# Optimization experiments

Measured on AMD Instinct MI355X. Metric: run time of the kernel, lower is better.

## Reference

```python
import jax, jax.numpy as jnp
import numpy as np

B, L, H, F, K, NBINS, T = 32, 512, 512, 512, 3, 256, 4096
EPS = 1e-8  # RMSNorm epsilon
PAD = (K - 1) // 2  # =1, matches both conv paddings in the torch module


def _conv1d(x, w, b):
    # x: [B, L, Cin], w: [K, Cin, Cout]
    return jax.lax.conv_general_dilated(
        x, w, window_strides=(1,), padding=[(PAD, PAD)],
        dimension_numbers=('NLC', 'LIO', 'NLC')) + b


def _rms(x, g):
    return g * x / (jnp.sqrt(jnp.mean(x * x, axis=-1, keepdims=True)) + EPS)


def _vpred(x, mask, w1, b1, g1, w2, b2, g2, wl, bl):
    h = _rms(jax.nn.relu(_conv1d(x, w1, b1)), g1)
    h = _rms(jax.nn.relu(_conv1d(h, w2, b2)), g2)
    out = (h @ wl + bl)[..., 0]  # [B, L]
    return jnp.where(mask, 0.0, out)


def _proj(x, w1, b1, w2, b2):
    return jax.nn.relu(jax.nn.relu(x @ w1 + b1) @ w2 + b2)


def _length_regulate(x, dur, max_len):
    # Vectorized equivalent of LengthRegulator: repeat phoneme i dur[b,i] times, pad to max_len.
    cum = jnp.cumsum(dur, axis=1)               # [B, L]
    mel_len = cum[:, -1]                        # [B]
    t = jnp.arange(max_len)                     # [T]
    idx = jax.vmap(lambda c: jnp.searchsorted(c, t, side='right'))(cum)  # [B, T]
    idx = jnp.minimum(idx, x.shape[1] - 1)
    out = jnp.take_along_axis(x, idx[:, :, None], axis=1)  # [B, T, H]
    valid = (t[None, :] < mel_len[:, None])
    return out * valid[:, :, None].astype(x.dtype), mel_len


def setup_inputs() -> dict:
    key = jax.random.key(0)
    ks = iter(jax.random.split(key, 64))
    n = lambda *s: jax.random.normal(next(ks), s, jnp.float32) * 0.05
    inp = {}
    inp['x'] = jax.random.normal(next(ks), (B, L, H), jnp.float32)
    inp['embedding'] = jax.random.normal(next(ks), (B, L, H), jnp.float32)
    inp['src_mask'] = jnp.zeros((B, L), bool)
    inp['duration_target'] = jax.random.randint(next(ks), (B, L), 0, 9, jnp.int32)
    inp['pitch_target'] = jax.random.normal(next(ks), (B, L), jnp.float32)
    inp['energy_target'] = jax.random.normal(next(ks), (B, L), jnp.float32)
    inp['max_len'] = T
    for p in ['dur', 'pit', 'eng']:
        inp[p + '_w1'] = n(K, H, F); inp[p + '_b1'] = jnp.zeros(F, jnp.float32)
        inp[p + '_g1'] = jnp.ones(F, jnp.float32)
        inp[p + '_w2'] = n(K, F, F); inp[p + '_b2'] = jnp.zeros(F, jnp.float32)
        inp[p + '_g2'] = jnp.ones(F, jnp.float32)
        inp[p + '_wl'] = n(F, 1); inp[p + '_bl'] = jnp.zeros(1, jnp.float32)
    for p in ['pp', 'ep', 'sp']:
        inp[p + '_w1'] = n(H, H); inp[p + '_b1'] = jnp.zeros(H, jnp.float32)
        inp[p + '_w2'] = n(H, H); inp[p + '_b2'] = jnp.zeros(H, jnp.float32)
    inp['pitch_bins'] = jnp.linspace(-3.0, 3.0, NBINS - 1)
    inp['energy_bins'] = jnp.linspace(-3.0, 3.0, NBINS - 1)
    inp['pitch_emb'] = n(NBINS, H)
    inp['energy_emb'] = n(NBINS, H)
    return inp


def reference(x, embedding, src_mask, duration_target, pitch_target, energy_target, max_len,
              dur_w1, dur_b1, dur_g1, dur_w2, dur_b2, dur_g2, dur_wl, dur_bl,
              pit_w1, pit_b1, pit_g1, pit_w2, pit_b2, pit_g2, pit_wl, pit_bl,
              eng_w1, eng_b1, eng_g1, eng_w2, eng_b2, eng_g2, eng_wl, eng_bl,
              pp_w1, pp_b1, pp_w2, pp_b2,
              ep_w1, ep_b1, ep_w2, ep_b2,
              sp_w1, sp_b1, sp_w2, sp_b2,
              pitch_bins, energy_bins, pitch_emb, energy_emb):
    log_dur = _vpred(x, src_mask, dur_w1, dur_b1, dur_g1, dur_w2, dur_b2, dur_g2, dur_wl, dur_bl)
    pit_pred = _vpred(x + _proj(embedding, pp_w1, pp_b1, pp_w2, pp_b2), src_mask,
                      pit_w1, pit_b1, pit_g1, pit_w2, pit_b2, pit_g2, pit_wl, pit_bl)
    pitch_embedding = pitch_emb[jnp.searchsorted(pitch_bins, pitch_target)]  # torch.bucketize right=False == side='left'
    eng_pred = _vpred(x + _proj(embedding, ep_w1, ep_b1, ep_w2, ep_b2), src_mask,
                      eng_w1, eng_b1, eng_g1, eng_w2, eng_b2, eng_g2, eng_wl, eng_bl)
    energy_embedding = energy_emb[jnp.searchsorted(energy_bins, energy_target)]
    xo = x + energy_embedding + pitch_embedding + _proj(embedding, sp_w1, sp_b1, sp_w2, sp_b2)
    out, mel_len = _length_regulate(xo, duration_target, max_len)
    return (out, pit_pred, eng_pred, log_dur, mel_len)
```

## Files before the change

### kernel.cpp

```cpp
#include <hip/hip_runtime.h>

#define Bv    32
#define Lv    512
#define Hv    512
#define Fv    512
#define Tv    4096
#define Mv    (Bv*Lv)
#define NBINSv 256

#define OUT_OFF 0
#define PIT_OFF (Bv*(size_t)Tv*Hv)
#define ENG_OFF (PIT_OFF + Mv)
#define DUR_OFF (ENG_OFF + Mv)
#define MEL_OFF (DUR_OFF + Mv)

typedef unsigned short ushort;
typedef __attribute__((ext_vector_type(8))) short   bf16x8;
typedef __attribute__((ext_vector_type(4))) float   f32x4;
typedef __attribute__((ext_vector_type(8))) unsigned short u16x8;

__device__ __forceinline__ float b2f(ushort u) {
    union { float f; unsigned u; } x; x.u = ((unsigned)u) << 16; return x.f;
}
__device__ __forceinline__ ushort f2b(float f) {
    union { float f; unsigned u; } x; x.f = f;
    unsigned r = x.u + 0x7fffu + ((x.u >> 16) & 1u);
    return (ushort)(r >> 16);
}

#define GLL16(g, l) __builtin_amdgcn_global_load_lds( \
    (const __attribute__((address_space(1))) void*)(g), \
    (__attribute__((address_space(3))) void*)(l), 16, 0, 0)

template<int NZ> struct GArgs {
    const ushort* A[NZ];
    const ushort* W[NZ];
    const float*  bias[NZ];
    ushort*       C[NZ];
};
struct EpiArgs {
    float* rss; const float* inv1; float* ss2; float* sgw;
    const float* g2[3]; const float* wl[3];
};
struct TransArgs { const float* src[6]; const float* gs[6]; ushort* dst[6]; };
struct ConvArgs  { const float* src[2]; ushort* dst[2]; };

template<int NTAPS, int EPI, int NZ>
__global__ __launch_bounds__(256) void gemm_bf16_kernel(
    GArgs<NZ> ga, EpiArgs ea, const float* __restrict__ res,
    const float* __restrict__ pe, const float* __restrict__ ee,
    const int* __restrict__ idxp, const int* __restrict__ idxe,
    const ushort* __restrict__ zp)
{
    constexpr int KTOT = NTAPS * 512;
    constexpr int GX   = Fv / 128;
    constexpr int GY   = Mv / 128;
    constexpr int NWG  = GX * GY * NZ;

    int lin = blockIdx.x + GX * (blockIdx.y + GY * blockIdx.z);
    lin = (lin & 7) * (NWG >> 3) + (lin >> 3);
    const int bx = lin & (GX - 1);
    const int by = (lin >> 2) & (GY - 1);
    const int z  = (NZ > 1) ? (lin / (GX * GY)) : 0;

    const ushort* __restrict__ A    = ga.A[z];
    const ushort* __restrict__ Bt   = ga.W[z];
    const float*  __restrict__ bias = ga.bias[z];
    ushort*       __restrict__ C    = ga.C[z];

    __shared__ ushort As[128 * 32];
    __shared__ ushort Bs[128 * 32];

    const int tid = threadIdx.x;
    const int n0 = bx * 128;
    const int m0 = by * 128;

    const int sar = tid >> 2;
    const int sl  = tid & 3;

    const int lane = tid & 63;
    const int w    = tid >> 6;
    const int wm   = (w & 1) * 64;
    const int wn   = (w >> 1) * 64;
    const int lr   = lane & 15;
    const int q    = lane >> 4;

    f32x4 acc[4][4];
    #pragma unroll
    for (int i = 0; i < 4; ++i)
        #pragma unroll
        for (int j = 0; j < 4; ++j) {
            f32x4 zz = {0.f, 0.f, 0.f, 0.f};
            acc[i][j] = zz;
        }

    for (int kt = 0; kt < NTAPS * 16; ++kt) {
        const int tap = (NTAPS == 3) ? (kt >> 4) : 0;
        const int kin = (NTAPS == 3) ? ((kt & 15) << 5) : (kt << 5);

        #pragma unroll
        for (int r = 0; r < 2; ++r) {
            const int row = sar + r * 64;
            const int m   = m0 + row;
            const int qg  = (sl - (row >> 1)) & 3;
            const ushort* asrc;
            if (NTAPS == 3) {
                const int l  = m & (Lv - 1);
                const int ls = l + tap - 1;
                asrc = ((unsigned)ls < (unsigned)Lv)
                     ? A + (size_t)(m + tap - 1) * 512 + kin + qg * 8
                     : zp;
            } else {
                asrc = A + (size_t)m * 512 + kin + qg * 8;
            }
            GLL16(asrc, &As[row * 32 + sl * 8]);
            const ushort* bsrc = Bt + (size_t)(n0 + row) * KTOT + tap * 512 + kin + qg * 8;
            GLL16(bsrc, &Bs[row * 32 + sl * 8]);
        }
        __syncthreads();

        bf16x8 af[4], bfr[4];
        #pragma unroll
        for (int i = 0; i < 4; ++i) {
            const int rm = wm + i * 16 + lr;
            af[i]  = *(const bf16x8*)&As[rm * 32 + (((q + (rm >> 1)) & 3) << 3)];
            const int rn = wn + i * 16 + lr;
            bfr[i] = *(const bf16x8*)&Bs[rn * 32 + (((q + (rn >> 1)) & 3) << 3)];
        }
        #pragma unroll
        for (int i = 0; i < 4; ++i)
            #pragma unroll
            for (int j = 0; j < 4; ++j)
                acc[i][j] = __builtin_amdgcn_mfma_f32_16x16x32_bf16(
                                af[i], bfr[j], acc[i][j], 0, 0, 0);
        __syncthreads();
    }

    int epi = EPI;
    if (EPI == 3) epi = (z == 2) ? 2 : 1;
    #pragma unroll
    for (int i = 0; i < 4; ++i) {
        #pragma unroll
        for (int r = 0; r < 4; ++r) {
            const int m = m0 + wm + i * 16 + q * 4 + r;
            const size_t ro = (size_t)m * 512;
            int ip = 0, ie = 0;
            if (EPI == 3 && epi == 2) { ip = idxp[m]; ie = idxe[m]; }
            float rowinv = 1.f;
            if (EPI == 5) rowinv = ea.inv1[(size_t)z * Mv + m];
            float ssp = 0.f, sgwp = 0.f;
            #pragma unroll
            for (int j = 0; j < 4; ++j) {
                const int n = n0 + wn + j * 16 + lr;
                float v = (EPI == 5) ? (acc[i][j][r] * rowinv + bias[n])
                                     : (acc[i][j][r] + bias[n]);
                v = fmaxf(v, 0.f);
                if (EPI == 3) v += res[ro + n];
                if (EPI == 3 && epi == 2)
                    v += pe[(size_t)ip * 512 + n] + ee[(size_t)ie * 512 + n];
                if (EPI != 5) C[ro + n] = f2b(v);
                if (EPI == 4) ssp += v * v;
                if (EPI == 5) { ssp += v * v; sgwp += v * ea.g2[z][n] * ea.wl[z][n]; }
            }
            if (EPI == 4 || EPI == 5) {
                #pragma unroll
                for (int mm = 1; mm < 16; mm <<= 1) {
                    ssp += __shfl_xor(ssp, mm, 64);
                    if (EPI == 5) sgwp += __shfl_xor(sgwp, mm, 64);
                }
                if (lr == 0) {
                    if (EPI == 4) atomicAdd(&ea.rss[(size_t)z * Mv + m], ssp);
                    if (EPI == 5) {
                        atomicAdd(&ea.ss2[(size_t)z * Mv + m], ssp);
                        atomicAdd(&ea.sgw[(size_t)z * Mv + m], sgwp);
                    }
                }
            }
        }
    }
}

__global__ __launch_bounds__(256) void convert_kernel(ConvArgs ca)
{
    const float* __restrict__ X  = ca.src[blockIdx.y];
    ushort*      __restrict__ Xb = ca.dst[blockIdx.y];
    const size_t i = (size_t)blockIdx.x * 256 + threadIdx.x;
    const float4 a = ((const float4*)X)[2 * i];
    const float4 b = ((const float4*)X)[2 * i + 1];
    u16x8 o;
    o[0] = f2b(a.x); o[1] = f2b(a.y); o[2] = f2b(a.z); o[3] = f2b(a.w);
    o[4] = f2b(b.x); o[5] = f2b(b.y); o[6] = f2b(b.z); o[7] = f2b(b.w);
    *(u16x8*)(Xb + i * 8) = o;
}

__global__ __launch_bounds__(256) void transpose_kernel(TransArgs ta, int Ktot)
{
    const float* __restrict__ W  = ta.src[blockIdx.z];
    const float* __restrict__ gs = ta.gs[blockIdx.z];
    ushort*      __restrict__ Wt = ta.dst[blockIdx.z];
    __shared__ float t[32][33];
    const int k0 = blockIdx.x * 32, n0 = blockIdx.y * 32;
    const int r = threadIdx.x >> 5, c = threadIdx.x & 31;
    #pragma unroll
    for (int rr = 0; rr < 4; ++rr) {
        const int kk = k0 + r + rr * 8;
        float v = W[(size_t)kk * 512 + n0 + c];
        if (gs) v *= gs[kk & 511];
        t[r + rr * 8][c] = v;
    }
    __syncthreads();
    #pragma unroll
    for (int rr = 0; rr < 4; ++rr)
        Wt[(size_t)(n0 + r + rr * 8) * Ktot + k0 + c] = f2b(t[c][r + rr * 8]);
}

__global__ __launch_bounds__(256) void finv_kernel(
    const float* __restrict__ rss, float* __restrict__ inv1)
{
    const int i = blockIdx.x * 256 + threadIdx.x;
    inv1[i] = 1.f / (sqrtf(rss[i] * (1.f / 512.f)) + 1e-8f);
}

__global__ __launch_bounds__(256) void pred_kernel(
    const float* __restrict__ ss2, const float* __restrict__ sgw,
    const unsigned char* __restrict__ mask,
    const float* __restrict__ bl0, const float* __restrict__ bl1,
    const float* __restrict__ bl2, float* __restrict__ predbase)
{
    const int i = blockIdx.x * 256 + threadIdx.x;
    const int zz = i >> 14;
    const int row = i & (Mv - 1);
    const float bl = (zz == 0 ? bl0 : (zz == 1 ? bl1 : bl2))[0];
    const float inv = 1.f / (sqrtf(ss2[i] * (1.f / 512.f)) + 1e-8f);
    predbase[i] = mask[row] ? 0.f : (sgw[i] * inv + bl);
}

__global__ __launch_bounds__(256) void idx_kernel(
    const float* __restrict__ pt, const float* __restrict__ et,
    const float* __restrict__ pbins, const float* __restrict__ ebins,
    int* __restrict__ idxp, int* __restrict__ idxe)
{
    __shared__ float pb[NBINSv - 1], ebn[NBINSv - 1];
    const int tid = threadIdx.x;
    if (tid < NBINSv - 1) { pb[tid] = pbins[tid]; ebn[tid] = ebins[tid]; }
    __syncthreads();
    const int m = blockIdx.x * 256 + tid;
    const float pv = pt[m], ev = et[m];
    int lo = 0, hi = NBINSv - 1;
    while (lo < hi) { int mid = (lo + hi) >> 1; if (pb[mid] < pv) lo = mid + 1; else hi = mid; }
    idxp[m] = lo;
    lo = 0; hi = NBINSv - 1;
    while (lo < hi) { int mid = (lo + hi) >> 1; if (ebn[mid] < ev) lo = mid + 1; else hi = mid; }
    idxe[m] = lo;
}

__global__ __launch_bounds__(512) void cumsum_kernel(
    const int* __restrict__ dur, int* __restrict__ cum,
    int* __restrict__ melint, float* __restrict__ melout)
{
    __shared__ int s[Lv];
    const int b = blockIdx.x, tid = threadIdx.x;
    s[tid] = dur[b * Lv + tid];
    __syncthreads();
    for (int off = 1; off < Lv; off <<= 1) {
        int t = (tid >= off) ? s[tid - off] : 0;
        __syncthreads();
        s[tid] += t;
        __syncthreads();
    }
    cum[b * Lv + tid] = s[tid];
    if (tid == Lv - 1) { melint[b] = s[tid]; melout[b] = (float)s[tid]; }
}

__global__ __launch_bounds__(256) void tmap_kernel(
    const int* __restrict__ cum, const int* __restrict__ melint,
    int* __restrict__ tmap)
{
    const int bt = blockIdx.x * 256 + threadIdx.x;
    const int b = bt >> 12;
    const int t = bt & (Tv - 1);
    const int* c = cum + b * Lv;
    int lo = 0, hi = Lv;
    while (lo < hi) { int mid = (lo + hi) >> 1; if (c[mid] <= t) lo = mid + 1; else hi = mid; }
    tmap[bt] = (t < melint[b]) ? (b * Lv + min(lo, Lv - 1)) : -1;
}

__global__ __launch_bounds__(128) void regulate_kernel(
    const ushort* __restrict__ xo, const int* __restrict__ tmap,
    float* __restrict__ out)
{
    const int bt = blockIdx.x;
    const int src = tmap[bt];
    float4 v = make_float4(0.f, 0.f, 0.f, 0.f);
    if (src >= 0) {
        const ushort4 u = ((const ushort4*)(xo + (size_t)src * 512))[threadIdx.x];
        v.x = b2f(u.x); v.y = b2f(u.y); v.z = b2f(u.z); v.w = b2f(u.w);
    }
    ((float4*)(out + (size_t)bt * 512))[threadIdx.x] = v;
}

extern "C" void kernel_launch(void* const* d_in, const int* in_sizes, int n_in,
                              void* d_out, int out_size, void* d_ws, size_t ws_size,
                              hipStream_t stream)
{
    const float* x    = (const float*)d_in[0];
    const float* emb  = (const float*)d_in[1];
    const unsigned char* mask = (const unsigned char*)d_in[2];
    const int*   durt = (const int*)d_in[3];
    const float* pt   = (const float*)d_in[4];
    const float* et   = (const float*)d_in[5];
    const float* dw1 = (const float*)d_in[7],  *db1 = (const float*)d_in[8],
               * dg1 = (const float*)d_in[9],  *dw2 = (const float*)d_in[10],
               * db2 = (const float*)d_in[11], *dg2 = (const float*)d_in[12],
               * dwl = (const float*)d_in[13], *dbl = (const float*)d_in[14];
    const float* pw1 = (const float*)d_in[15], *pb1 = (const float*)d_in[16],
               * pg1 = (const float*)d_in[17], *pw2 = (const float*)d_in[18],
               * pb2 = (const float*)d_in[19], *pg2 = (const float*)d_in[20],
               * pwl = (const float*)d_in[21], *pbl = (const float*)d_in[22];
    const float* ew1 = (const float*)d_in[23], *eb1 = (const float*)d_in[24],
               * eg1 = (const float*)d_in[25], *ew2 = (const float*)d_in[26],
               * eb2 = (const float*)d_in[27], *eg2 = (const float*)d_in[28],
               * ewl = (const float*)d_in[29], *ebl = (const float*)d_in[30];
    const float* ppw1 = (const float*)d_in[31], *ppb1 = (const float*)d_in[32],
               * ppw2 = (const float*)d_in[33], *ppb2 = (const float*)d_in[34];
    const float* epw1 = (const float*)d_in[35], *epb1 = (const float*)d_in[36],
               * epw2 = (const float*)d_in[37], *epb2 = (const float*)d_in[38];
    const float* spw1 = (const float*)d_in[39], *spb1 = (const float*)d_in[40],
               * spw2 = (const float*)d_in[41], *spb2 = (const float*)d_in[42];
    const float* pbins = (const float*)d_in[43];
    const float* ebins = (const float*)d_in[44];
    const float* pemb  = (const float*)d_in[45];
    const float* eemb  = (const float*)d_in[46];

    float* outf = (float*)d_out;

    int*    cum    = (int*)d_ws;
    int*    melint = cum + 16384;
    int*    idxp   = melint + 64;
    int*    idxe   = idxp + 16384;
    ushort* zp     = (ushort*)(idxe + 16384);
    int*    tmap   = idxe + 16448;
    ushort* xob    = (ushort*)((float*)d_ws + 262144);

    #define OBUF(i) ((ushort*)(outf + (size_t)(i) * 4194304))
    ushort* xb  = OBUF(0);   ushort* eb  = OBUF(1);
    ushort* pA0 = OBUF(2);   ushort* pA1 = OBUF(3);  ushort* pA2 = OBUF(4);
    ushort* xp  = OBUF(5);   ushort* xe  = OBUF(6);
    ushort* c0  = OBUF(7);   ushort* c1  = OBUF(8);  ushort* c2  = OBUF(9);
    float*  rss  = outf + 10ull * 4194304;
    float*  ss2  = rss + 3 * Mv;
    float*  sgw  = rss + 6 * Mv;
    float*  inv1 = rss + 9 * Mv;
    ushort* wt[12];
    {
        size_t off = 13ull * 4194304;
        for (int i = 0; i < 6; ++i)  { wt[i] = (ushort*)(outf + off); off += 393216; }
        for (int i = 6; i < 12; ++i) { wt[i] = (ushort*)(outf + off); off += 131072; }
    }

    hipMemsetAsync(zp, 0, 64, stream);
    hipMemsetAsync(rss, 0, 9ull * Mv * sizeof(float), stream);

    { ConvArgs ca = {{x, emb}, {xb, eb}};
      convert_kernel<<<dim3(4096, 2), 256, 0, stream>>>(ca); }
    { TransArgs ta = {{dw1, dw2, pw1, pw2, ew1, ew2},
                      {nullptr, dg1, nullptr, pg1, nullptr, eg1},
                      {wt[0], wt[1], wt[2], wt[3], wt[4], wt[5]}};
      transpose_kernel<<<dim3(48, 16, 6), 256, 0, stream>>>(ta, 1536); }
    { TransArgs ta = {{ppw1, ppw2, epw1, epw2, spw1, spw2},
                      {nullptr, nullptr, nullptr, nullptr, nullptr, nullptr},
                      {wt[6], wt[7], wt[8], wt[9], wt[10], wt[11]}};
      transpose_kernel<<<dim3(16, 16, 6), 256, 0, stream>>>(ta, 512); }

    idx_kernel<<<Mv / 256, 256, 0, stream>>>(pt, et, pbins, ebins, idxp, idxe);
    cumsum_kernel<<<Bv, Lv, 0, stream>>>(durt, cum, melint, outf + MEL_OFF);
    tmap_kernel<<<Bv * Tv / 256, 256, 0, stream>>>(cum, melint, tmap);

    const dim3 g3(Fv / 128, Mv / 128, 3);
    const EpiArgs eaN = {nullptr, nullptr, nullptr, nullptr,
                         {nullptr, nullptr, nullptr}, {nullptr, nullptr, nullptr}};

    { GArgs<3> a = {{eb, eb, eb}, {wt[6], wt[8], wt[10]}, {ppb1, epb1, spb1}, {pA0, pA1, pA2}};
      gemm_bf16_kernel<1, 0, 3><<<g3, 256, 0, stream>>>(a, eaN, nullptr, nullptr, nullptr,
                                                        nullptr, nullptr, zp); }
    { GArgs<3> a = {{pA0, pA1, pA2}, {wt[7], wt[9], wt[11]}, {ppb2, epb2, spb2}, {xp, xe, xob}};
      gemm_bf16_kernel<1, 3, 3><<<g3, 256, 0, stream>>>(a, eaN, x, pemb, eemb,
                                                        idxp, idxe, zp); }

    { GArgs<3> a = {{xp, xe, xb}, {wt[2], wt[4], wt[0]}, {pb1, eb1, db1}, {c0, c1, c2}};
      EpiArgs ea = eaN; ea.rss = rss;
      gemm_bf16_kernel<3, 4, 3><<<g3, 256, 0, stream>>>(a, ea, nullptr, nullptr, nullptr,
                                                        nullptr, nullptr, zp); }
    finv_kernel<<<3 * Mv / 256, 256, 0, stream>>>(rss, inv1);
    { GArgs<3> a = {{c0, c1, c2}, {wt[3], wt[5], wt[1]}, {pb2, eb2, db2}, {c0, c1, c2}};
      EpiArgs ea = {nullptr, inv1, ss2, sgw, {pg2, eg2, dg2}, {pwl, ewl, dwl}};
      gemm_bf16_kernel<3, 5, 3><<<g3, 256, 0, stream>>>(a, ea, nullptr, nullptr, nullptr,
                                                        nullptr, nullptr, zp); }
    pred_kernel<<<3 * Mv / 256, 256, 0, stream>>>(ss2, sgw, mask, pbl, ebl, dbl,
                                                  outf + PIT_OFF);

    regulate_kernel<<<Bv * Tv, 128, 0, stream>>>(xob, tmap, outf + OUT_OFF);
}
```

Baseline: 795.6 us.

## Run variance-predictor conv GEMMs in FP8 with fused inverse-RMS and tmap

The two 3-tap conv GEMMs of the three variance predictors now take FP8 (e4m3) activations and weights and use the fp8 MFMA instruction. The producing epilogues and the weight transpose write FP8, which halves operand bytes. The separate finv kernel is folded into the second GEMM's epilogue, and the cumsum and tmap kernels are merged into one. The risk is lower precision in the predictions from FP8 quantization of unscaled activations, which may exceed tolerance.

```diff
diff --git a/kernel.cpp b/kernel.cpp
--- a/kernel.cpp
+++ b/kernel.cpp
@@ -15,6 +15,7 @@
 #define MEL_OFF (DUR_OFF + Mv)
 
 typedef unsigned short ushort;
+typedef unsigned char  uchar;
 typedef __attribute__((ext_vector_type(8))) short   bf16x8;
 typedef __attribute__((ext_vector_type(4))) float   f32x4;
 typedef __attribute__((ext_vector_type(8))) unsigned short u16x8;
@@ -26,6 +27,15 @@
     union { float f; unsigned u; } x; x.f = f;
     unsigned r = x.u + 0x7fffu + ((x.u >> 16) & 1u);
     return (ushort)(r >> 16);
+}
+__device__ __forceinline__ uchar f2e4(float f) {
+    int r = __builtin_amdgcn_cvt_pk_fp8_f32(f, 0.f, 0, false);
+    return (uchar)(r & 0xff);
+}
+__device__ __forceinline__ int pk4e4(float v0, float v1, float v2, float v3) {
+    int r = __builtin_amdgcn_cvt_pk_fp8_f32(v0, v1, 0, false);
+    r     = __builtin_amdgcn_cvt_pk_fp8_f32(v2, v3, r, true);
+    return r;
 }
 
 #define GLL16(g, l) __builtin_amdgcn_global_load_lds( \
@@ -38,16 +48,21 @@
     const float*  bias[NZ];
     ushort*       C[NZ];
 };
+template<int NZ> struct GArgs8 {
+    const uchar* A[NZ];
+    const uchar* W[NZ];
+    const float* bias[NZ];
+    uchar*       C[NZ];
+};
 struct EpiArgs {
-    float* rss; const float* inv1; float* ss2; float* sgw;
+    float* rss; float* ss2; float* sgw;
     const float* g2[3]; const float* wl[3];
 };
-struct TransArgs { const float* src[6]; const float* gs[6]; ushort* dst[6]; };
-struct ConvArgs  { const float* src[2]; ushort* dst[2]; };
+struct TransArgs { const float* src[6]; const float* gs[6]; void* dst[6]; };
 
 template<int NTAPS, int EPI, int NZ>
 __global__ __launch_bounds__(256) void gemm_bf16_kernel(
-    GArgs<NZ> ga, EpiArgs ea, const float* __restrict__ res,
+    GArgs<NZ> ga, const float* __restrict__ res,
     const float* __restrict__ pe, const float* __restrict__ ee,
     const int* __restrict__ idxp, const int* __restrict__ idxe,
     const ushort* __restrict__ zp)
@@ -136,8 +151,7 @@
         __syncthreads();
     }
 
-    int epi = EPI;
-    if (EPI == 3) epi = (z == 2) ? 2 : 1;
+    uchar* C8 = (uchar*)C;
     #pragma unroll
     for (int i = 0; i < 4; ++i) {
         #pragma unroll
@@ -145,9 +159,109 @@
             const int m = m0 + wm + i * 16 + q * 4 + r;
             const size_t ro = (size_t)m * 512;
             int ip = 0, ie = 0;
-            if (EPI == 3 && epi == 2) { ip = idxp[m]; ie = idxe[m]; }
+            if (EPI == 3 && z == 2) { ip = idxp[m]; ie = idxe[m]; }
+            #pragma unroll
+            for (int j = 0; j < 4; ++j) {
+                const int n = n0 + wn + j * 16 + lr;
+                float v = acc[i][j][r] + bias[n];
+                v = fmaxf(v, 0.f);
+                if (EPI == 3) v += res[ro + n];
+                if (EPI == 3 && z == 2)
+                    v += pe[(size_t)ip * 512 + n] + ee[(size_t)ie * 512 + n];
+                if (EPI == 3 && z < 2) C8[ro + n] = f2e4(v);
+                else                   C[ro + n]  = f2b(v);
+            }
+        }
+    }
+}
+
+template<int EPI, int NZ>
+__global__ __launch_bounds__(256) void gemm_fp8_kernel(
+    GArgs8<NZ> ga, EpiArgs ea, const uchar* __restrict__ zp)
+{
+    constexpr int GX = 4, GY = 128, NWG = GX * GY * NZ;
+
+    int lin = blockIdx.x + GX * (blockIdx.y + GY * blockIdx.z);
+    lin = (lin & 7) * (NWG >> 3) + (lin >> 3);
+    const int bx = lin & (GX - 1);
+    const int by = (lin >> 2) & (GY - 1);
+    const int z  = (NZ > 1) ? (lin / (GX * GY)) : 0;
+
+    const uchar* __restrict__ A    = ga.A[z];
+    const uchar* __restrict__ Bt   = ga.W[z];
+    const float* __restrict__ bias = ga.bias[z];
+    uchar*       __restrict__ C    = ga.C[z];
+
+    __shared__ long Asl[512];
+    __shared__ long Bsl[512];
+    uchar* As = (uchar*)Asl;
+    uchar* Bs = (uchar*)Bsl;
+
+    const int tid = threadIdx.x;
+    const int n0 = bx * 128;
+    const int m0 = by * 128;
+
+    const int sar = tid >> 1;
+    const int sl  = tid & 1;
+
+    const int lane = tid & 63;
+    const int w    = tid >> 6;
+    const int wm   = (w & 1) * 64;
+    const int wn   = (w >> 1) * 64;
+    const int lr   = lane & 15;
+    const int q    = lane >> 4;
+
+    f32x4 acc[4][4];
+    #pragma unroll
+    for (int i = 0; i < 4; ++i)
+        #pragma unroll
+        for (int j = 0; j < 4; ++j) {
+            f32x4 zz = {0.f, 0.f, 0.f, 0.f};
+            acc[i][j] = zz;
+        }
+
+    const int gs = (sl ^ ((sar >> 2) & 1)) << 4;
+    for (int kt = 0; kt < 48; ++kt) {
+        const int tap = kt >> 4;
+        const int kin = (kt & 15) << 5;
+        {
+            const int m  = m0 + sar;
+            const int ls = (m & (Lv - 1)) + tap - 1;
+            const uchar* asrc = ((unsigned)ls < (unsigned)Lv)
+                ? A + (size_t)(m + tap - 1) * 512 + kin + gs
+                : zp;
+            GLL16(asrc, &As[sar * 32 + sl * 16]);
+            const uchar* bsrc = Bt + (size_t)(n0 + sar) * 1536 + tap * 512 + kin + gs;
+            GLL16(bsrc, &Bs[sar * 32 + sl * 16]);
+        }
+        __syncthreads();
+
+        long af[4], bf[4];
+        #pragma unroll
+        for (int i = 0; i < 4; ++i) {
+            const int rm = wm + i * 16 + lr;
+            af[i] = *(const long*)&As[rm * 32 + (((q >> 1) ^ ((rm >> 2) & 1)) << 4) + ((q & 1) << 3)];
+            const int rn = wn + i * 16 + lr;
+            bf[i] = *(const long*)&Bs[rn * 32 + (((q >> 1) ^ ((rn >> 2) & 1)) << 4) + ((q & 1) << 3)];
+        }
+        #pragma unroll
+        for (int i = 0; i < 4; ++i)
+            #pragma unroll
+            for (int j = 0; j < 4; ++j)
+                acc[i][j] = __builtin_amdgcn_mfma_f32_16x16x32_fp8_fp8(
+                                af[i], bf[j], acc[i][j], 0, 0, 0);
+        __syncthreads();
+    }
+
+    #pragma unroll
+    for (int i = 0; i < 4; ++i) {
+        #pragma unroll
+        for (int r = 0; r < 4; ++r) {
+            const int m = m0 + wm + i * 16 + q * 4 + r;
+            const size_t ro = (size_t)m * 512;
             float rowinv = 1.f;
-            if (EPI == 5) rowinv = ea.inv1[(size_t)z * Mv + m];
+            if (EPI == 5)
+                rowinv = 1.f / (sqrtf(ea.rss[(size_t)z * Mv + m] * (1.f / 512.f)) + 1e-8f);
             float ssp = 0.f, sgwp = 0.f;
             #pragma unroll
             for (int j = 0; j < 4; ++j) {
@@ -155,49 +269,52 @@
                 float v = (EPI == 5) ? (acc[i][j][r] * rowinv + bias[n])
                                      : (acc[i][j][r] + bias[n]);
                 v = fmaxf(v, 0.f);
-                if (EPI == 3) v += res[ro + n];
-                if (EPI == 3 && epi == 2)
-                    v += pe[(size_t)ip * 512 + n] + ee[(size_t)ie * 512 + n];
-                if (EPI != 5) C[ro + n] = f2b(v);
-                if (EPI == 4) ssp += v * v;
-                if (EPI == 5) { ssp += v * v; sgwp += v * ea.g2[z][n] * ea.wl[z][n]; }
+                if (EPI == 4) { C[ro + n] = f2e4(v); ssp += v * v; }
+                else          { ssp += v * v; sgwp += v * ea.g2[z][n] * ea.wl[z][n]; }
             }
-            if (EPI == 4 || EPI == 5) {
-                #pragma unroll
-                for (int mm = 1; mm < 16; mm <<= 1) {
-                    ssp += __shfl_xor(ssp, mm, 64);
-                    if (EPI == 5) sgwp += __shfl_xor(sgwp, mm, 64);
-                }
-                if (lr == 0) {
-                    if (EPI == 4) atomicAdd(&ea.rss[(size_t)z * Mv + m], ssp);
-                    if (EPI == 5) {
-                        atomicAdd(&ea.ss2[(size_t)z * Mv + m], ssp);
-                        atomicAdd(&ea.sgw[(size_t)z * Mv + m], sgwp);
-                    }
+            #pragma unroll
+            for (int mm = 1; mm < 16; mm <<= 1) {
+                ssp += __shfl_xor(ssp, mm, 64);
+                if (EPI == 5) sgwp += __shfl_xor(sgwp, mm, 64);
+            }
+            if (lr == 0) {
+                if (EPI == 4) atomicAdd(&ea.rss[(size_t)z * Mv + m], ssp);
+                else {
+                    atomicAdd(&ea.ss2[(size_t)z * Mv + m], ssp);
+                    atomicAdd(&ea.sgw[(size_t)z * Mv + m], sgwp);
                 }
             }
         }
     }
 }
 
-__global__ __launch_bounds__(256) void convert_kernel(ConvArgs ca)
-{
-    const float* __restrict__ X  = ca.src[blockIdx.y];
-    ushort*      __restrict__ Xb = ca.dst[blockIdx.y];
+__global__ __launch_bounds__(256) void convert_kernel(
+    const float* __restrict__ x, const float* __restrict__ emb,
+    uchar* __restrict__ xb8, ushort* __restrict__ eb)
+{
     const size_t i = (size_t)blockIdx.x * 256 + threadIdx.x;
-    const float4 a = ((const float4*)X)[2 * i];
-    const float4 b = ((const float4*)X)[2 * i + 1];
-    u16x8 o;
-    o[0] = f2b(a.x); o[1] = f2b(a.y); o[2] = f2b(a.z); o[3] = f2b(a.w);
-    o[4] = f2b(b.x); o[5] = f2b(b.y); o[6] = f2b(b.z); o[7] = f2b(b.w);
-    *(u16x8*)(Xb + i * 8) = o;
-}
-
+    if (blockIdx.y == 0) {
+        const float4 a = ((const float4*)x)[2 * i];
+        const float4 b = ((const float4*)x)[2 * i + 1];
+        int2 o;
+        o.x = pk4e4(a.x, a.y, a.z, a.w);
+        o.y = pk4e4(b.x, b.y, b.z, b.w);
+        ((int2*)xb8)[i] = o;
+    } else {
+        const float4 a = ((const float4*)emb)[2 * i];
+        const float4 b = ((const float4*)emb)[2 * i + 1];
+        u16x8 o;
+        o[0] = f2b(a.x); o[1] = f2b(a.y); o[2] = f2b(a.z); o[3] = f2b(a.w);
+        o[4] = f2b(b.x); o[5] = f2b(b.y); o[6] = f2b(b.z); o[7] = f2b(b.w);
+        *(u16x8*)(eb + i * 8) = o;
+    }
+}
+
+template<int FP8>
 __global__ __launch_bounds__(256) void transpose_kernel(TransArgs ta, int Ktot)
 {
     const float* __restrict__ W  = ta.src[blockIdx.z];
     const float* __restrict__ gs = ta.gs[blockIdx.z];
-    ushort*      __restrict__ Wt = ta.dst[blockIdx.z];
     __shared__ float t[32][33];
     const int k0 = blockIdx.x * 32, n0 = blockIdx.y * 32;
     const int r = threadIdx.x >> 5, c = threadIdx.x & 31;
@@ -210,15 +327,11 @@
     }
     __syncthreads();
     #pragma unroll
-    for (int rr = 0; rr < 4; ++rr)
-        Wt[(size_t)(n0 + r + rr * 8) * Ktot + k0 + c] = f2b(t[c][r + rr * 8]);
-}
-
-__global__ __launch_bounds__(256) void finv_kernel(
-    const float* __restrict__ rss, float* __restrict__ inv1)
-{
-    const int i = blockIdx.x * 256 + threadIdx.x;
-    inv1[i] = 1.f / (sqrtf(rss[i] * (1.f / 512.f)) + 1e-8f);
+    for (int rr = 0; rr < 4; ++rr) {
+        const size_t o = (size_t)(n0 + r + rr * 8) * Ktot + k0 + c;
+        if (FP8) ((uchar*)ta.dst[blockIdx.z])[o]  = f2e4(t[c][r + rr * 8]);
+        else     ((ushort*)ta.dst[blockIdx.z])[o] = f2b(t[c][r + rr * 8]);
+    }
 }
 
 __global__ __launch_bounds__(256) void pred_kernel(
@@ -254,9 +367,9 @@
     idxe[m] = lo;
 }
 
-__global__ __launch_bounds__(512) void cumsum_kernel(
-    const int* __restrict__ dur, int* __restrict__ cum,
-    int* __restrict__ melint, float* __restrict__ melout)
+__global__ __launch_bounds__(512) void cumtmap_kernel(
+    const int* __restrict__ dur, float* __restrict__ melout,
+    int* __restrict__ tmap)
 {
     __shared__ int s[Lv];
     const int b = blockIdx.x, tid = threadIdx.x;
@@ -268,21 +381,13 @@
         s[tid] += t;
         __syncthreads();
     }
-    cum[b * Lv + tid] = s[tid];
-    if (tid == Lv - 1) { melint[b] = s[tid]; melout[b] = (float)s[tid]; }
-}
-
-__global__ __launch_bounds__(256) void tmap_kernel(
-    const int* __restrict__ cum, const int* __restrict__ melint,
-    int* __restrict__ tmap)
-{
-    const int bt = blockIdx.x * 256 + threadIdx.x;
-    const int b = bt >> 12;
-    const int t = bt & (Tv - 1);
-    const int* c = cum + b * Lv;
-    int lo = 0, hi = Lv;
-    while (lo < hi) { int mid = (lo + hi) >> 1; if (c[mid] <= t) lo = mid + 1; else hi = mid; }
-    tmap[bt] = (t < melint[b]) ? (b * Lv + min(lo, Lv - 1)) : -1;
+    const int mel = s[Lv - 1];
+    if (tid == Lv - 1) melout[b] = (float)mel;
+    for (int t = tid; t < Tv; t += Lv) {
+        int lo = 0, hi = Lv;
+        while (lo < hi) { int mid = (lo + hi) >> 1; if (s[mid] <= t) lo = mid + 1; else hi = mid; }
+        tmap[b * Tv + t] = (t < mel) ? (b * Lv + min(lo, Lv - 1)) : -1;
+    }
 }
 
 __global__ __launch_bounds__(128) void regulate_kernel(
@@ -343,59 +448,60 @@
     ushort* xob    = (ushort*)((float*)d_ws + 262144);
 
     #define OBUF(i) ((ushort*)(outf + (size_t)(i) * 4194304))
-    ushort* xb  = OBUF(0);   ushort* eb  = OBUF(1);
+    uchar*  xb8 = (uchar*)OBUF(0);
+    ushort* eb  = OBUF(1);
     ushort* pA0 = OBUF(2);   ushort* pA1 = OBUF(3);  ushort* pA2 = OBUF(4);
-    ushort* xp  = OBUF(5);   ushort* xe  = OBUF(6);
-    ushort* c0  = OBUF(7);   ushort* c1  = OBUF(8);  ushort* c2  = OBUF(9);
+    uchar*  xp8 = (uchar*)OBUF(5);
+    uchar*  xe8 = (uchar*)OBUF(6);
+    uchar*  c8_0 = (uchar*)OBUF(7);
+    uchar*  c8_1 = (uchar*)OBUF(8);
+    uchar*  c8_2 = (uchar*)OBUF(9);
     float*  rss  = outf + 10ull * 4194304;
     float*  ss2  = rss + 3 * Mv;
     float*  sgw  = rss + 6 * Mv;
-    float*  inv1 = rss + 9 * Mv;
-    ushort* wt[12];
+    uchar*  w8[6];
+    ushort* wt[6];
     {
         size_t off = 13ull * 4194304;
-        for (int i = 0; i < 6; ++i)  { wt[i] = (ushort*)(outf + off); off += 393216; }
-        for (int i = 6; i < 12; ++i) { wt[i] = (ushort*)(outf + off); off += 131072; }
+        for (int i = 0; i < 6; ++i) { w8[i] = (uchar*)(outf + off); off += 196608; }
+        for (int i = 0; i < 6; ++i) { wt[i] = (ushort*)(outf + off); off += 131072; }
     }
 
     hipMemsetAsync(zp, 0, 64, stream);
     hipMemsetAsync(rss, 0, 9ull * Mv * sizeof(float), stream);
 
-    { ConvArgs ca = {{x, emb}, {xb, eb}};
-      convert_kernel<<<dim3(4096, 2), 256, 0, stream>>>(ca); }
+    convert_kernel<<<dim3(4096, 2), 256, 0, stream>>>(x, emb, xb8, eb);
     { TransArgs ta = {{dw1, dw2, pw1, pw2, ew1, ew2},
                       {nullptr, dg1, nullptr, pg1, nullptr, eg1},
-                      {wt[0], wt[1], wt[2], wt[3], wt[4], wt[5]}};
-      transpose_kernel<<<dim3(48, 16, 6), 256, 0, stream>>>(ta, 1536); }
+                      {w8[0], w8[1], w8[2], w8[3], w8[4], w8[5]}};
+      transpose_kernel<1><<<dim3(48, 16, 6), 256, 0, stream>>>(ta, 1536); }
     { TransArgs ta = {{ppw1, ppw2, epw1, epw2, spw1, spw2},
                       {nullptr, nullptr, nullptr, nullptr, nullptr, nullptr},
-                      {wt[6], wt[7], wt[8], wt[9], wt[10], wt[11]}};
-      transpose_kernel<<<dim3(16, 16, 6), 256, 0, stream>>>(ta, 512); }
+                      {wt[0], wt[1], wt[2], wt[3], wt[4], wt[5]}};
+      transpose_kernel<0><<<dim3(16, 16, 6), 256, 0, stream>>>(ta, 512); }
 
     idx_kernel<<<Mv / 256, 256, 0, stream>>>(pt, et, pbins, ebins, idxp, idxe);
-    cumsum_kernel<<<Bv, Lv, 0, stream>>>(durt, cum, melint, outf + MEL_OFF);
-    tmap_kernel<<<Bv * Tv / 256, 256, 0, stream>>>(cum, melint, tmap);
+    cumtmap_kernel<<<Bv, Lv, 0, stream>>>(durt, outf + MEL_OFF, tmap);
 
     const dim3 g3(Fv / 128, Mv / 128, 3);
-    const EpiArgs eaN = {nullptr, nullptr, nullptr, nullptr,
-                         {nullptr, nullptr, nullptr}, {nullptr, nullptr, nullptr}};
-
-    { GArgs<3> a = {{eb, eb, eb}, {wt[6], wt[8], wt[10]}, {ppb1, epb1, spb1}, {pA0, pA1, pA2}};
-      gemm_bf16_kernel<1, 0, 3><<<g3, 256, 0, stream>>>(a, eaN, nullptr, nullptr, nullptr,
+
+    { GArgs<3> a = {{eb, eb, eb}, {wt[0], wt[2], wt[4]}, {ppb1, epb1, spb1}, {pA0, pA1, pA2}};
+      gemm_bf16_kernel<1, 0, 3><<<g3, 256, 0, stream>>>(a, nullptr, nullptr, nullptr,
                                                         nullptr, nullptr, zp); }
-    { GArgs<3> a = {{pA0, pA1, pA2}, {wt[7], wt[9], wt[11]}, {ppb2, epb2, spb2}, {xp, xe, xob}};
-      gemm_bf16_kernel<1, 3, 3><<<g3, 256, 0, stream>>>(a, eaN, x, pemb, eemb,
+    { GArgs<3> a = {{pA0, pA1, pA2}, {wt[1], wt[3], wt[5]}, {ppb2, epb2, spb2},
+                    {(ushort*)xp8, (ushort*)xe8, xob}};
+      gemm_bf16_kernel<1, 3, 3><<<g3, 256, 0, stream>>>(a, x, pemb, eemb,
                                                         idxp, idxe, zp); }
 
-    { GArgs<3> a = {{xp, xe, xb}, {wt[2], wt[4], wt[0]}, {pb1, eb1, db1}, {c0, c1, c2}};
-      EpiArgs ea = eaN; ea.rss = rss;
-      gemm_bf16_kernel<3, 4, 3><<<g3, 256, 0, stream>>>(a, ea, nullptr, nullptr, nullptr,
-                                                        nullptr, nullptr, zp); }
-    finv_kernel<<<3 * Mv / 256, 256, 0, stream>>>(rss, inv1);
-    { GArgs<3> a = {{c0, c1, c2}, {wt[3], wt[5], wt[1]}, {pb2, eb2, db2}, {c0, c1, c2}};
-      EpiArgs ea = {nullptr, inv1, ss2, sgw, {pg2, eg2, dg2}, {pwl, ewl, dwl}};
-      gemm_bf16_kernel<3, 5, 3><<<g3, 256, 0, stream>>>(a, ea, nullptr, nullptr, nullptr,
-                                                        nullptr, nullptr, zp); }
+    { GArgs8<3> a = {{xp8, xe8, xb8}, {w8[2], w8[4], w8[0]}, {pb1, eb1, db1},
+                     {c8_0, c8_1, c8_2}};
+      EpiArgs ea = {rss, nullptr, nullptr, {nullptr, nullptr, nullptr},
+                    {nullptr, nullptr, nullptr}};
+      gemm_fp8_kernel<4, 3><<<g3, 256, 0, stream>>>(a, ea, (const uchar*)zp); }
+    { GArgs8<3> a = {{c8_0, c8_1, c8_2}, {w8[3], w8[5], w8[1]}, {pb2, eb2, db2},
+                     {c8_0, c8_1, c8_2}};
+      EpiArgs ea = {rss, ss2, sgw, {pg2, eg2, dg2}, {pwl, ewl, dwl}};
+      gemm_fp8_kernel<5, 3><<<g3, 256, 0, stream>>>(a, ea, (const uchar*)zp); }
     pred_kernel<<<3 * Mv / 256, 256, 0, stream>>>(ss2, sgw, mask, pbl, ebl, dbl,
                                                   outf + PIT_OFF);
 
```

After: 864.3 us. 1.09x slower.
